# Kernel optimization log

Measured on AMD Instinct MI355X. Metric: run time of the kernel, lower is better.

Reference implementation:

```python
import jax, jax.numpy as jnp
import numpy as np

N_DRUG, N_GENE = 20000, 40000
D_DRUG, D_GENE = 128, 64
HID, EMB = 64, 32
E_DD, E_DG, E_GG = 1500000, 1000000, 1500000


def setup_inputs() -> dict:
    key = jax.random.key(0)
    ks = iter(jax.random.split(key, 32))

    def nrm(shape, scale=0.05):
        return jax.random.normal(next(ks), shape, dtype=jnp.float32) * scale

    def idx(n, e):
        return jax.random.randint(next(ks), (e,), 0, n, dtype=jnp.int32)

    return dict(
        feat_drug=nrm((N_DRUG, D_DRUG), 1.0),
        feat_gene=nrm((N_GENE, D_GENE), 1.0),
        dd_src=idx(N_DRUG, E_DD), dd_dst=idx(N_DRUG, E_DD),
        dg_src=idx(N_DRUG, E_DG), dg_dst=idx(N_GENE, E_DG),
        gg_src=idx(N_GENE, E_GG), gg_dst=idx(N_GENE, E_GG),
        neg_src=idx(N_DRUG, E_DD), neg_dst=idx(N_DRUG, E_DD),
        W1_dd=nrm((D_DRUG, HID)), W1_dg=nrm((D_DRUG, HID)), W1_gg=nrm((D_GENE, HID)),
        W1_self_drug=nrm((D_DRUG, HID)), W1_self_gene=nrm((D_GENE, HID)),
        b1=jnp.zeros((HID,), jnp.float32),
        W2_dd=nrm((HID, EMB)), W2_dg=nrm((HID, EMB)), W2_gg=nrm((HID, EMB)),
        W2_self_drug=nrm((HID, EMB)), W2_self_gene=nrm((HID, EMB)),
        b2=jnp.zeros((EMB,), jnp.float32),
        w_rel=nrm((EMB,), 1.0),
    )


def _mean_agg(msg_nodes, src, dst, n_dst):
    # transform-then-gather: msg_nodes is [n_src, out]; gather per edge, scatter-sum to dst,
    # divide by dst in-degree (DGL GraphConv norm='right').
    m = jax.ops.segment_sum(msg_nodes[src], dst, num_segments=n_dst)
    deg = jax.ops.segment_sum(jnp.ones(dst.shape, msg_nodes.dtype), dst, num_segments=n_dst)
    return m / jnp.clip(deg, 1.0)[:, None]


def _rel_layer(hd, hg, edges, Wdd, Wdg, Wgg, Wsd, Wsg, b, act):
    dd_src, dd_dst, dg_src, dg_dst, gg_src, gg_dst = edges
    # per-relation linear transform on src nodes, then mean aggregation to dst;
    # sum across relations sharing the same dst node type (HeteroGraphConv aggregate='sum')
    agg_d = _mean_agg(hd @ Wdd, dd_src, dd_dst, hd.shape[0])
    agg_g = (_mean_agg(hd @ Wdg, dg_src, dg_dst, hg.shape[0])
             + _mean_agg(hg @ Wgg, gg_src, gg_dst, hg.shape[0]))
    out_d = agg_d + hd @ Wsd + b  # self-loop + bias
    out_g = agg_g + hg @ Wsg + b
    if act:
        out_d, out_g = jax.nn.relu(out_d), jax.nn.relu(out_g)
    return out_d, out_g


def reference(feat_drug, feat_gene, dd_src, dd_dst, dg_src, dg_dst, gg_src, gg_dst,
              neg_src, neg_dst, W1_dd, W1_dg, W1_gg, W1_self_drug, W1_self_gene, b1,
              W2_dd, W2_dg, W2_gg, W2_self_drug, W2_self_gene, b2, w_rel):
    edges = (dd_src, dd_dst, dg_src, dg_dst, gg_src, gg_dst)
    h_d, h_g = _rel_layer(feat_drug, feat_gene, edges,
                          W1_dd, W1_dg, W1_gg, W1_self_drug, W1_self_gene, b1, True)
    h_d, h_g = _rel_layer(h_d, h_g, edges,
                          W2_dd, W2_dg, W2_gg, W2_self_drug, W2_self_gene, b2, False)
    # per-edge-type diagonal-bilinear dot-product scorer, etype='dd' (drug-drug)
    pos = jnp.sum(h_d[dd_src] * w_rel * h_d[dd_dst], axis=-1)
    neg = jnp.sum(h_d[neg_src] * w_rel * h_d[neg_dst], axis=-1)
    return pos, neg
```

## Files before the change

kernel.cpp:

```cpp
#include <hip/hip_runtime.h>


#define NPART 8

template<int KIN>
__global__ __launch_bounds__(256) void gemm_reg_kernel(const float* __restrict__ A,
                                                       const float* __restrict__ W,
                                                       float* __restrict__ out, int M) {
    const int lane = threadIdx.x & 63;
    const int gwave = blockIdx.x * (blockDim.x >> 6) + (threadIdx.x >> 6);
    const int nwave = gridDim.x * (blockDim.x >> 6);
    float w[KIN];
#pragma unroll
    for (int k = 0; k < KIN; ++k) w[k] = W[k * 64 + lane];
    for (int m0 = gwave * 2; m0 < M; m0 += nwave * 2) {
        const int mu = __builtin_amdgcn_readfirstlane(m0);
        const float* a0 = A + (size_t)mu * KIN;
        const float* a1 = a0 + KIN;
        const bool two = (mu + 1) < M;
        float acc0 = 0.0f, acc1 = 0.0f;
#pragma unroll
        for (int k = 0; k < KIN; ++k) {
            const float av0 = a0[k];
            const float av1 = two ? a1[k] : 0.0f;
            acc0 = fmaf(av0, w[k], acc0);
            acc1 = fmaf(av1, w[k], acc1);
        }
        out[(size_t)mu * 64 + lane] = acc0;
        if (two) out[(size_t)(mu + 1) * 64 + lane] = acc1;
    }
}

__global__ __launch_bounds__(256) void gemm2_reg_kernel(const float* __restrict__ A,
                                                        const float* __restrict__ Wa,
                                                        const float* __restrict__ Wb,
                                                        float* __restrict__ out_a,
                                                        float* __restrict__ out_b, int M) {
    const int lane = threadIdx.x & 63;
    const int col = lane & 31;
    const float* Wm = (lane < 32) ? Wa : Wb;
    float* om = (lane < 32) ? out_a : out_b;
    const int gwave = blockIdx.x * (blockDim.x >> 6) + (threadIdx.x >> 6);
    const int nwave = gridDim.x * (blockDim.x >> 6);
    float w[64];
#pragma unroll
    for (int k = 0; k < 64; ++k) w[k] = Wm[k * 32 + col];
    for (int m0 = gwave * 2; m0 < M; m0 += nwave * 2) {
        const int mu = __builtin_amdgcn_readfirstlane(m0);
        const float* a0 = A + (size_t)mu * 64;
        const float* a1 = a0 + 64;
        const bool two = (mu + 1) < M;
        float acc0 = 0.0f, acc1 = 0.0f;
#pragma unroll
        for (int k = 0; k < 64; ++k) {
            const float av0 = a0[k];
            const float av1 = two ? a1[k] : 0.0f;
            acc0 = fmaf(av0, w[k], acc0);
            acc1 = fmaf(av1, w[k], acc1);
        }
        om[(size_t)mu * 32 + col] = acc0;
        if (two) om[(size_t)(mu + 1) * 32 + col] = acc1;
    }
}

__global__ __launch_bounds__(256) void degree_part_kernel(const int* __restrict__ dst,
                                                          int* __restrict__ deg,
                                                          int E, int psz) {
    const int part = blockIdx.x & (NPART - 1);
    const int lo = part * psz, hi = lo + psz;
    const int bpp = gridDim.x >> 3;
    const int bip = blockIdx.x >> 3;
    const int stride = bpp * 256;
    for (int e = bip * 256 + threadIdx.x; e < E; e += stride) {
        const int d = dst[e];
        if (d >= lo && d < hi) atomicAdd(&deg[d], 1);
    }
}

__global__ __launch_bounds__(1024) void scan_kernel(const int* __restrict__ deg,
                                                    int* __restrict__ off,
                                                    int* __restrict__ cursor, int N) {
    __shared__ int part[1024];
    const int t = threadIdx.x;
    const int per = (N + 1023) / 1024;
    const int beg = t * per;
    const int end = min(beg + per, N);
    int s = 0;
    for (int i = beg; i < end; ++i) s += deg[i];
    part[t] = s;
    __syncthreads();
    for (int d = 1; d < 1024; d <<= 1) {
        int v = (t >= d) ? part[t - d] : 0;
        __syncthreads();
        part[t] += v;
        __syncthreads();
    }
    int run = (t == 0) ? 0 : part[t - 1];
    for (int i = beg; i < end; ++i) { off[i] = run; cursor[i] = run; run += deg[i]; }
    if (t == 1023) off[N] = part[1023];
}

__global__ __launch_bounds__(256) void fill_part_kernel(const int* __restrict__ src,
                                                        const int* __restrict__ dst,
                                                        int* __restrict__ cursor,
                                                        int* __restrict__ csr_src,
                                                        int E, int psz) {
    const int part = blockIdx.x & (NPART - 1);
    const int lo = part * psz, hi = lo + psz;
    const int bpp = gridDim.x >> 3;
    const int bip = blockIdx.x >> 3;
    const int stride = bpp * 256;
    for (int e = bip * 256 + threadIdx.x; e < E; e += stride) {
        const int d = dst[e];
        const int s = src[e];
        if (d >= lo && d < hi) {
            const int p = atomicAdd(&cursor[d], 1);
            csr_src[p] = s;
        }
    }
}

template<int W, bool RELU>
__global__ __launch_bounds__(256) void gather_combine_kernel(
        const float* __restrict__ msg, const int* __restrict__ csr_src,
        const int* __restrict__ off, const int* __restrict__ endp,
        const float* __restrict__ selfb, const float* __restrict__ b,
        float* __restrict__ out, int N) {
    const int GRP = 256 / W;
    const int g = threadIdx.x / W;
    const int lane = threadIdx.x % W;
    const float bk = b[lane];
    for (int n = blockIdx.x * GRP + g; n < N; n += gridDim.x * GRP) {
        const int beg = off[n], end = endp[n];
        float acc = 0.0f;
        int i = beg;
        for (; i + 4 <= end; i += 4) {
            const int s0 = csr_src[i], s1 = csr_src[i + 1];
            const int s2 = csr_src[i + 2], s3 = csr_src[i + 3];
            const float v0 = msg[(size_t)s0 * W + lane];
            const float v1 = msg[(size_t)s1 * W + lane];
            const float v2 = msg[(size_t)s2 * W + lane];
            const float v3 = msg[(size_t)s3 * W + lane];
            acc += (v0 + v1) + (v2 + v3);
        }
        for (; i < end; ++i) acc += msg[(size_t)csr_src[i] * W + lane];
        const float d = (end > beg) ? (float)(end - beg) : 1.0f;
        float v = acc / d + selfb[(size_t)n * W + lane] + bk;
        if (RELU) v = fmaxf(v, 0.0f);
        out[(size_t)n * W + lane] = v;
    }
}

__global__ __launch_bounds__(256) void score2_kernel(const float* __restrict__ h,
                                                     const int* __restrict__ sA,
                                                     const int* __restrict__ dA,
                                                     const int* __restrict__ sB,
                                                     const int* __restrict__ dB,
                                                     const float* __restrict__ wrel,
                                                     float* __restrict__ outA,
                                                     float* __restrict__ outB,
                                                     int EA, int EB) {
    const int lj = threadIdx.x & 7;
    const size_t grp = ((size_t)blockIdx.x * blockDim.x + threadIdx.x) >> 3;
    const size_t ngrp = ((size_t)gridDim.x * blockDim.x) >> 3;
    const float4 w = *(const float4*)(wrel + lj * 4);
    const size_t total = (size_t)EA + (size_t)EB;
    for (size_t e = grp; e < total; e += ngrp) {
        int s, d; float* o;
        if (e < (size_t)EA) { s = sA[e]; d = dA[e]; o = outA + e; }
        else { const size_t e2 = e - EA; s = sB[e2]; d = dB[e2]; o = outB + e2; }
        const float4 hs = *(const float4*)(h + (size_t)s * 32 + lj * 4);
        const float4 hd = *(const float4*)(h + (size_t)d * 32 + lj * 4);
        float p = hs.x * w.x * hd.x + hs.y * w.y * hd.y +
                  hs.z * w.z * hd.z + hs.w * w.w * hd.w;
        p += __shfl_xor(p, 1, 64);
        p += __shfl_xor(p, 2, 64);
        p += __shfl_xor(p, 4, 64);
        if (lj == 0) *o = p;
    }
}

extern "C" void kernel_launch(void* const* d_in, const int* in_sizes, int n_in,
                              void* d_out, int out_size, void* d_ws, size_t ws_size,
                              hipStream_t stream) {
    const float* feat_drug    = (const float*)d_in[0];
    const int*   dd_src       = (const int*)d_in[2];
    const int*   dd_dst       = (const int*)d_in[3];
    const int*   neg_src      = (const int*)d_in[8];
    const int*   neg_dst      = (const int*)d_in[9];
    const float* W1_dd        = (const float*)d_in[10];
    const float* W1_self_drug = (const float*)d_in[13];
    const float* b1           = (const float*)d_in[15];
    const float* W2_dd        = (const float*)d_in[16];
    const float* W2_self_drug = (const float*)d_in[19];
    const float* b2           = (const float*)d_in[21];
    const float* w_rel        = (const float*)d_in[22];

    const int N  = in_sizes[0] / 128;
    const int E  = in_sizes[2];
    const int EN = in_sizes[8];
    const int PSZ = (N + NPART - 1) / NPART;

    char* ws = (char*)d_ws;
    int*   deg_i   = (int*)ws;                         ws += (size_t)N * 4;
    int*   off     = (int*)ws;                         ws += (size_t)(N + 1) * 4;
    int*   cursor  = (int*)ws;                         ws += (size_t)(N + 1) * 4;
    int*   csr_src = (int*)ws;                         ws += (size_t)E * 4;
    float* msg1    = (float*)ws;                       ws += (size_t)N * 64 * 4;
    float* self1   = (float*)ws;                       ws += (size_t)N * 64 * 4;
    float* h1      = (float*)ws;                       ws += (size_t)N * 64 * 4;
    float* msg2    = (float*)ws;                       ws += (size_t)N * 32 * 4;
    float* self2   = (float*)ws;                       ws += (size_t)N * 32 * 4;
    float* h2      = (float*)ws;                       ws += (size_t)N * 32 * 4;

    float* pos = (float*)d_out;
    float* neg = pos + E;

    hipMemsetAsync(deg_i, 0, (size_t)N * sizeof(int), stream);

    degree_part_kernel<<<512, 256, 0, stream>>>(dd_dst, deg_i, E, PSZ);
    scan_kernel<<<1, 1024, 0, stream>>>(deg_i, off, cursor, N);
    fill_part_kernel<<<512, 256, 0, stream>>>(dd_src, dd_dst, cursor, csr_src, E, PSZ);

    gemm_reg_kernel<128><<<512, 256, 0, stream>>>(feat_drug, W1_dd, msg1, N);
    gemm_reg_kernel<128><<<512, 256, 0, stream>>>(feat_drug, W1_self_drug, self1, N);
    gather_combine_kernel<64, true><<<(N + 3) / 4, 256, 0, stream>>>(
        msg1, csr_src, off, cursor, self1, b1, h1, N);

    gemm2_reg_kernel<<<512, 256, 0, stream>>>(h1, W2_dd, W2_self_drug, msg2, self2, N);
    gather_combine_kernel<32, false><<<(N + 7) / 8, 256, 0, stream>>>(
        msg2, csr_src, off, cursor, self2, b2, h2, N);

    score2_kernel<<<4096, 256, 0, stream>>>(h2, dd_src, dd_dst, neg_src, neg_dst,
                                            w_rel, pos, neg, E, EN);
}
```

Measured before the change: 424.8 us.

## Build CSR from per-edge-chunk degree/cursor copies instead of dst-range partition

Instead of having each of 8 block partitions scan all edges and keep only destinations in their range, the edge list is split into 8 chunks, and each chunk keeps its own degree and cursor arrays. This removes the 8x redundant reads of dst and spreads atomic contention across separate copies. The cost is a scan over 8N entries in a single-block kernel, plus 8 offset pairs per node in the gather kernels, which adds index loads and splits each node's neighbor list into segments.

```diff
diff --git a/kernel.cpp b/kernel.cpp
--- a/kernel.cpp
+++ b/kernel.cpp
@@ -63,28 +63,27 @@
     }
 }
 
-__global__ __launch_bounds__(256) void degree_part_kernel(const int* __restrict__ dst,
-                                                          int* __restrict__ deg,
-                                                          int E, int psz) {
-    const int part = blockIdx.x & (NPART - 1);
-    const int lo = part * psz, hi = lo + psz;
-    const int bpp = gridDim.x >> 3;
+__global__ __launch_bounds__(256) void degree8_kernel(const int* __restrict__ dst,
+                                                      int* __restrict__ deg8,
+                                                      int E, int chunk, int N) {
+    const int p = blockIdx.x & (NPART - 1);
+    const int lo = p * chunk;
+    const int hi = min(lo + chunk, E);
+    int* __restrict__ deg = deg8 + (size_t)p * N;
     const int bip = blockIdx.x >> 3;
-    const int stride = bpp * 256;
-    for (int e = bip * 256 + threadIdx.x; e < E; e += stride) {
-        const int d = dst[e];
-        if (d >= lo && d < hi) atomicAdd(&deg[d], 1);
-    }
+    const int stride = (gridDim.x >> 3) * 256;
+    for (int e = lo + bip * 256 + threadIdx.x; e < hi; e += stride)
+        atomicAdd(&deg[dst[e]], 1);
 }
 
 __global__ __launch_bounds__(1024) void scan_kernel(const int* __restrict__ deg,
                                                     int* __restrict__ off,
-                                                    int* __restrict__ cursor, int N) {
+                                                    int* __restrict__ cursor, int M8) {
     __shared__ int part[1024];
     const int t = threadIdx.x;
-    const int per = (N + 1023) / 1024;
+    const int per = (M8 + 1023) / 1024;
     const int beg = t * per;
-    const int end = min(beg + per, N);
+    const int end = min(beg + per, M8);
     int s = 0;
     for (int i = beg; i < end; ++i) s += deg[i];
     part[t] = s;
@@ -97,33 +96,32 @@
     }
     int run = (t == 0) ? 0 : part[t - 1];
     for (int i = beg; i < end; ++i) { off[i] = run; cursor[i] = run; run += deg[i]; }
-    if (t == 1023) off[N] = part[1023];
-}
-
-__global__ __launch_bounds__(256) void fill_part_kernel(const int* __restrict__ src,
-                                                        const int* __restrict__ dst,
-                                                        int* __restrict__ cursor,
-                                                        int* __restrict__ csr_src,
-                                                        int E, int psz) {
-    const int part = blockIdx.x & (NPART - 1);
-    const int lo = part * psz, hi = lo + psz;
-    const int bpp = gridDim.x >> 3;
+    if (t == 1023) off[M8] = part[1023];
+}
+
+__global__ __launch_bounds__(256) void fill8_kernel(const int* __restrict__ src,
+                                                    const int* __restrict__ dst,
+                                                    int* __restrict__ cursor8,
+                                                    int* __restrict__ csr_src,
+                                                    int E, int chunk, int N) {
+    const int p = blockIdx.x & (NPART - 1);
+    const int lo = p * chunk;
+    const int hi = min(lo + chunk, E);
+    int* __restrict__ cursor = cursor8 + (size_t)p * N;
     const int bip = blockIdx.x >> 3;
-    const int stride = bpp * 256;
-    for (int e = bip * 256 + threadIdx.x; e < E; e += stride) {
+    const int stride = (gridDim.x >> 3) * 256;
+    for (int e = lo + bip * 256 + threadIdx.x; e < hi; e += stride) {
         const int d = dst[e];
         const int s = src[e];
-        if (d >= lo && d < hi) {
-            const int p = atomicAdd(&cursor[d], 1);
-            csr_src[p] = s;
-        }
+        const int pos = atomicAdd(&cursor[d], 1);
+        csr_src[pos] = s;
     }
 }
 
 template<int W, bool RELU>
 __global__ __launch_bounds__(256) void gather_combine_kernel(
         const float* __restrict__ msg, const int* __restrict__ csr_src,
-        const int* __restrict__ off, const int* __restrict__ endp,
+        const int* __restrict__ off8, const int* __restrict__ end8,
         const float* __restrict__ selfb, const float* __restrict__ b,
         float* __restrict__ out, int N) {
     const int GRP = 256 / W;
@@ -131,20 +129,25 @@
     const int lane = threadIdx.x % W;
     const float bk = b[lane];
     for (int n = blockIdx.x * GRP + g; n < N; n += gridDim.x * GRP) {
-        const int beg = off[n], end = endp[n];
         float acc = 0.0f;
-        int i = beg;
-        for (; i + 4 <= end; i += 4) {
-            const int s0 = csr_src[i], s1 = csr_src[i + 1];
-            const int s2 = csr_src[i + 2], s3 = csr_src[i + 3];
-            const float v0 = msg[(size_t)s0 * W + lane];
-            const float v1 = msg[(size_t)s1 * W + lane];
-            const float v2 = msg[(size_t)s2 * W + lane];
-            const float v3 = msg[(size_t)s3 * W + lane];
-            acc += (v0 + v1) + (v2 + v3);
+        int cnt = 0;
+        for (int p = 0; p < NPART; ++p) {
+            const int beg = off8[(size_t)p * N + n];
+            const int end = end8[(size_t)p * N + n];
+            cnt += end - beg;
+            int i = beg;
+            for (; i + 4 <= end; i += 4) {
+                const int s0 = csr_src[i], s1 = csr_src[i + 1];
+                const int s2 = csr_src[i + 2], s3 = csr_src[i + 3];
+                const float v0 = msg[(size_t)s0 * W + lane];
+                const float v1 = msg[(size_t)s1 * W + lane];
+                const float v2 = msg[(size_t)s2 * W + lane];
+                const float v3 = msg[(size_t)s3 * W + lane];
+                acc += (v0 + v1) + (v2 + v3);
+            }
+            for (; i < end; ++i) acc += msg[(size_t)csr_src[i] * W + lane];
         }
-        for (; i < end; ++i) acc += msg[(size_t)csr_src[i] * W + lane];
-        const float d = (end > beg) ? (float)(end - beg) : 1.0f;
+        const float d = (cnt > 0) ? (float)cnt : 1.0f;
         float v = acc / d + selfb[(size_t)n * W + lane] + bk;
         if (RELU) v = fmaxf(v, 0.0f);
         out[(size_t)n * W + lane] = v;
@@ -199,12 +202,13 @@
     const int N  = in_sizes[0] / 128;
     const int E  = in_sizes[2];
     const int EN = in_sizes[8];
-    const int PSZ = (N + NPART - 1) / NPART;
+    const int CHUNK = (E + NPART - 1) / NPART;
+    const int M8 = NPART * N;
 
     char* ws = (char*)d_ws;
-    int*   deg_i   = (int*)ws;                         ws += (size_t)N * 4;
-    int*   off     = (int*)ws;                         ws += (size_t)(N + 1) * 4;
-    int*   cursor  = (int*)ws;                         ws += (size_t)(N + 1) * 4;
+    int*   deg8    = (int*)ws;                         ws += (size_t)M8 * 4;
+    int*   off8    = (int*)ws;                         ws += (size_t)(M8 + 1) * 4;
+    int*   cursor8 = (int*)ws;                         ws += (size_t)M8 * 4;
     int*   csr_src = (int*)ws;                         ws += (size_t)E * 4;
     float* msg1    = (float*)ws;                       ws += (size_t)N * 64 * 4;
     float* self1   = (float*)ws;                       ws += (size_t)N * 64 * 4;
@@ -216,20 +220,20 @@
     float* pos = (float*)d_out;
     float* neg = pos + E;
 
-    hipMemsetAsync(deg_i, 0, (size_t)N * sizeof(int), stream);
-
-    degree_part_kernel<<<512, 256, 0, stream>>>(dd_dst, deg_i, E, PSZ);
-    scan_kernel<<<1, 1024, 0, stream>>>(deg_i, off, cursor, N);
-    fill_part_kernel<<<512, 256, 0, stream>>>(dd_src, dd_dst, cursor, csr_src, E, PSZ);
+    hipMemsetAsync(deg8, 0, (size_t)M8 * sizeof(int), stream);
+
+    degree8_kernel<<<1024, 256, 0, stream>>>(dd_dst, deg8, E, CHUNK, N);
+    scan_kernel<<<1, 1024, 0, stream>>>(deg8, off8, cursor8, M8);
+    fill8_kernel<<<1024, 256, 0, stream>>>(dd_src, dd_dst, cursor8, csr_src, E, CHUNK, N);
 
     gemm_reg_kernel<128><<<512, 256, 0, stream>>>(feat_drug, W1_dd, msg1, N);
     gemm_reg_kernel<128><<<512, 256, 0, stream>>>(feat_drug, W1_self_drug, self1, N);
     gather_combine_kernel<64, true><<<(N + 3) / 4, 256, 0, stream>>>(
-        msg1, csr_src, off, cursor, self1, b1, h1, N);
+        msg1, csr_src, off8, cursor8, self1, b1, h1, N);
 
     gemm2_reg_kernel<<<512, 256, 0, stream>>>(h1, W2_dd, W2_self_drug, msg2, self2, N);
     gather_combine_kernel<32, false><<<(N + 7) / 8, 256, 0, stream>>>(
-        msg2, csr_src, off, cursor, self2, b2, h2, N);
+        msg2, csr_src, off8, cursor8, self2, b2, h2, N);
 
     score2_kernel<<<4096, 256, 0, stream>>>(h2, dd_src, dd_dst, neg_src, neg_dst,
                                             w_rel, pos, neg, E, EN);
```

Result: slower. 754.5 us (+77.6%).
